# Performance work log

Measured on AMD Instinct MI355X. Metric: run time of the kernel, lower is better.

Reference implementation:

```python
import jax, jax.numpy as jnp
import numpy as np

HIDDEN = 768
HEADS = 12
HEAD_DIM = HIDDEN // HEADS
SCALE = HEAD_DIM ** -0.5
B, S = 8, 1024


def _qkv(x, Wqkv):
    # x: [b, s, H] -> q, k, v each [b, heads, s, d]
    h = jnp.einsum('bsh,hk->bsk', x, Wqkv)          # [b, s, 3*H]
    h = h.reshape(x.shape[0], x.shape[1], 3, HEADS, HEAD_DIM)
    h = jnp.transpose(h, (2, 0, 3, 1, 4))           # [3, b, heads, s, d]
    return h[0], h[1], h[2]


def _attn(q, k, v):
    # q,k,v: [b, heads, s, d]
    att = jax.nn.softmax(jnp.einsum('bhxd,bhyd->bhxy', q, k) * SCALE, axis=-1)
    return jnp.einsum('bhxy,bhyd->bhxd', att, v)


def _out(o, Wout, bout):
    # o: [b, heads, s, d] -> [b, s, H]
    b, h, s, d = o.shape
    o = jnp.transpose(o, (0, 2, 1, 3)).reshape(b, s, h * d)
    return jnp.einsum('bsh,hk->bsk', o, Wout) + bout


def setup_inputs() -> dict:
    key = jax.random.key(0)
    k1, k2, k3, k4, k5 = jax.random.split(key, 5)
    x = jax.random.normal(k1, (B, S, HIDDEN), dtype=jnp.float32)
    x2 = jax.random.normal(k2, (B, S, HIDDEN), dtype=jnp.float32)
    Wqkv = jax.random.normal(k3, (HIDDEN, 3 * HIDDEN), dtype=jnp.float32) * (HIDDEN ** -0.5)
    Wout = jax.random.normal(k4, (HIDDEN, HIDDEN), dtype=jnp.float32) * (HIDDEN ** -0.5)
    bout = jax.random.normal(k5, (HIDDEN,), dtype=jnp.float32) * 0.01
    return {'x': x, 'x2': x2, 'Wqkv': Wqkv, 'Wout': Wout, 'bout': bout}


def reference(x, x2, Wqkv, Wout, bout):
    q, k, v = _qkv(x, Wqkv)
    q2, k2, v2 = _qkv(x2, Wqkv)
    o1 = _attn(q, k, v)      # self-attention on x
    o2 = _attn(q2, k2, v2)   # self-attention on x2
    o3 = _attn(q, k2, v2)    # cross-attention: queries from x, keys/values from x2
    y1 = _out(o1, Wout, bout)
    y2 = _out(o2, Wout, bout)
    y3 = _out(o3, Wout, bout)
    return (y1, y2, y3)
```

## Files before the change

### kernel.cpp

```cpp
#include <hip/hip_runtime.h>
#include <math.h>


#define HIDDEN 768
#define NH 12
#define HD 64
#define BB 8
#define SS 1024
#define ATT_SCALE 0.125f

typedef unsigned short u16;
typedef unsigned int u32;
typedef __attribute__((ext_vector_type(8))) short short8;
typedef __attribute__((ext_vector_type(4))) float f32x4;

constexpr int MROWS = BB * SS;
constexpr int M_QKV = 2 * MROWS;
constexpr int N_QKV = 3 * HIDDEN;
constexpr long QKV_ELEMS = (long)BB * NH * SS * HD;
constexpr long AX_ELEMS  = (long)M_QKV * HIDDEN;
constexpr long O_ELEMS   = (long)3 * MROWS * HIDDEN;
constexpr long WQT_ELEMS = (long)N_QKV * HIDDEN;
constexpr size_t OFF2 = (size_t)12 * QKV_ELEMS * 2;

__device__ inline u16 f2bf(float x) {
    u32 u = __float_as_uint(x);
    return (u16)((u + 0x7FFFu + ((u >> 16) & 1u)) >> 16);
}
__device__ inline float bf2f(u16 h) { return __uint_as_float(((u32)h) << 16); }
__device__ inline int swz(int row, int bcol) {
    return ((row << 7) + bcol) ^ ((row & 7) << 4);
}
__device__ inline int swzV(int row, int bcol) {
    return ((row << 7) + bcol) ^ ((((row >> 3) ^ row) & 7) << 4);
}
#define MFMA16(a, b, c) __builtin_amdgcn_mfma_f32_16x16x32_bf16(a, b, c, 0, 0, 0)

__device__ inline void gload16(const u16* g, u16* l) {
    __builtin_amdgcn_global_load_lds(
        (const __attribute__((address_space(1))) u32*)g,
        (__attribute__((address_space(3))) u32*)l, 16, 0, 0);
}

__global__ __launch_bounds__(256) void conv_x_kernel(
    const float* __restrict__ x, const float* __restrict__ x2,
    u16* __restrict__ axh, u16* __restrict__ axl)
{
    const size_t HALF = (size_t)MROWS * HIDDEN;
    const size_t NTOT = (size_t)AX_ELEMS;
    const size_t step = (size_t)gridDim.x * 256 * 4;
    for (size_t e = ((size_t)blockIdx.x * 256 + threadIdx.x) * 4; e < NTOT; e += step) {
        const float4 v = (e < HALF) ? *(const float4*)&x[e]
                                    : *(const float4*)&x2[e - HALF];
        ushort4 h, l;
        h.x = f2bf(v.x); l.x = f2bf(v.x - bf2f(h.x));
        h.y = f2bf(v.y); l.y = f2bf(v.y - bf2f(h.y));
        h.z = f2bf(v.z); l.z = f2bf(v.z - bf2f(h.z));
        h.w = f2bf(v.w); l.w = f2bf(v.w - bf2f(h.w));
        *(ushort4*)&axh[e] = h;
        *(ushort4*)&axl[e] = l;
    }
}

__global__ __launch_bounds__(256) void conv_wt_kernel(
    const float* __restrict__ Wqkv, const float* __restrict__ Wout,
    u16* __restrict__ wqt_h, u16* __restrict__ wqt_l,
    u16* __restrict__ wot_h, u16* __restrict__ wot_l)
{
    __shared__ float T[64][65];
    const int bk = blockIdx.x;
    int bn = blockIdx.y;
    const float* W; int ncols; u16 *oh, *ol;
    if (bn < 36) { W = Wqkv; ncols = N_QKV; oh = wqt_h; ol = wqt_l; }
    else         { W = Wout; ncols = HIDDEN; oh = wot_h; ol = wot_l; bn -= 36; }
    const int k0 = bk * 64, n0 = bn * 64;
    const int t = threadIdx.x;
    {
        const int r = t >> 2, c0 = (t & 3) * 16;
        #pragma unroll
        for (int q = 0; q < 4; ++q) {
            const float4 v = *(const float4*)&W[(size_t)(k0 + r) * ncols + n0 + c0 + q * 4];
            T[r][c0 + q * 4 + 0] = v.x;
            T[r][c0 + q * 4 + 1] = v.y;
            T[r][c0 + q * 4 + 2] = v.z;
            T[r][c0 + q * 4 + 3] = v.w;
        }
    }
    __syncthreads();
    {
        const int n = t >> 2, kk0 = (t & 3) * 16;
        const size_t ob = (size_t)(n0 + n) * HIDDEN + k0 + kk0;
        #pragma unroll
        for (int q = 0; q < 4; ++q) {
            ushort4 h, l;
            float v0 = T[kk0 + q * 4 + 0][n];
            float v1 = T[kk0 + q * 4 + 1][n];
            float v2 = T[kk0 + q * 4 + 2][n];
            float v3 = T[kk0 + q * 4 + 3][n];
            h.x = f2bf(v0); l.x = f2bf(v0 - bf2f(h.x));
            h.y = f2bf(v1); l.y = f2bf(v1 - bf2f(h.y));
            h.z = f2bf(v2); l.z = f2bf(v2 - bf2f(h.z));
            h.w = f2bf(v3); l.w = f2bf(v3 - bf2f(h.w));
            *(ushort4*)&oh[ob + q * 4] = h;
            *(ushort4*)&ol[ob + q * 4] = l;
        }
    }
}

__global__ __launch_bounds__(256)
__attribute__((amdgpu_waves_per_eu(2, 3)))
void gemm_qkv_mfma(const u16* __restrict__ Agh, const u16* __restrict__ Agl,
                   const u16* __restrict__ Bgh, const u16* __restrict__ Bgl,
                   u16* __restrict__ planes)
{
    __shared__ u16 LAh[4096], LAl[4096], LBh[4096], LBl[4096];

    const int tid = threadIdx.x, lane = tid & 63, wid = tid >> 6;
    const int l15 = lane & 15, lg = lane >> 4;
    const int wr = wid >> 1, wc = wid & 1;
    const int m0 = blockIdx.x * 128, n0 = blockIdx.y * 128;

    const f32x4 fz = {0.f, 0.f, 0.f, 0.f};
    f32x4 acc[4][4] = {{fz,fz,fz,fz},{fz,fz,fz,fz},{fz,fz,fz,fz},{fz,fz,fz,fz}};

    for (int kt = 0; kt < HIDDEN / 32; ++kt) {
        const int k0 = kt * 32;
        __syncthreads();
        #pragma unroll
        for (int u = 0; u < 2; ++u) {
            const int s   = (wid * 2 + u) * 64 + lane;
            const int row = s >> 2;
            const int kc  = (s & 3) * 8;
            const int lo  = (wid * 2 + u) * 512;
            const size_t ga = (size_t)(m0 + row) * HIDDEN + k0 + kc;
            const size_t gb = (size_t)(n0 + row) * HIDDEN + k0 + kc;
            gload16(Agh + ga, &LAh[lo]);
            gload16(Agl + ga, &LAl[lo]);
            gload16(Bgh + gb, &LBh[lo]);
            gload16(Bgl + gb, &LBl[lo]);
        }
        __syncthreads();

        short8 ah[4], al[4], bh[4], bl[4];
        #pragma unroll
        for (int i = 0; i < 4; ++i) {
            const int ro = (wr * 64 + i * 16 + l15) * 32 + lg * 8;
            ah[i] = *(const short8*)&LAh[ro];
            al[i] = *(const short8*)&LAl[ro];
        }
        #pragma unroll
        for (int j = 0; j < 4; ++j) {
            const int ro = (wc * 64 + j * 16 + l15) * 32 + lg * 8;
            bh[j] = *(const short8*)&LBh[ro];
            bl[j] = *(const short8*)&LBl[ro];
        }
        #pragma unroll
        for (int i = 0; i < 4; ++i)
            #pragma unroll
            for (int j = 0; j < 4; ++j) {
                acc[i][j] = MFMA16(ah[i], bh[j], acc[i][j]);
                acc[i][j] = MFMA16(ah[i], bl[j], acc[i][j]);
                acc[i][j] = MFMA16(al[i], bh[j], acc[i][j]);
            }
    }

    #pragma unroll
    for (int i = 0; i < 4; ++i) {
        #pragma unroll
        for (int r = 0; r < 4; ++r) {
            const int mr  = m0 + wr * 64 + i * 16 + lg * 4 + r;
            const int inp = (mr >= MROWS) ? 1 : 0;
            const int mm  = mr & (MROWS - 1);
            const int bb  = mm >> 10, ssr = mm & (SS - 1);
            #pragma unroll
            for (int j = 0; j < 4; ++j) {
                const int n   = n0 + wc * 64 + j * 16 + l15;
                const int sel = n / HIDDEN;
                const int hh  = (n % HIDDEN) >> 6;
                const int dd  = n & 63;
                const float v = acc[i][j][r];
                const u16 vh = f2bf(v);
                const u16 vl = f2bf(v - bf2f(vh));
                u16* ph = planes + (size_t)(inp * 6 + sel * 2) * QKV_ELEMS;
                const size_t idx = (((size_t)bb * NH + hh) * SS + ssr) * HD + dd;
                ph[idx] = vh;
                ph[QKV_ELEMS + idx] = vl;
            }
        }
    }
}

__global__ __launch_bounds__(256)
__attribute__((amdgpu_waves_per_eu(2, 2)))
void attn_mfma_kernel(const u16* __restrict__ planes,
                      u16* __restrict__ o_h, u16* __restrict__ o_l)
{
    __shared__ u16 Khi[64 * 64], Klo[64 * 64];
    __shared__ u16 Vthi[64 * 64], Vtlo[64 * 64];
    __shared__ u16 Pbuf[4][2][2][16 * 64];

    const int tid  = threadIdx.x;
    const int lane = tid & 63, wid = tid >> 6;
    const int l15  = lane & 15, lg = lane >> 4;

    const int work = (blockIdx.x & 7) * 288 + (blockIdx.x >> 3);
    const int qt   = work & 7;
    const int bh   = (work >> 3) % 96;
    const int aid  = (work >> 3) / 96;

    const int qinp  = (aid == 1) ? 1 : 0;
    const int kvinp = (aid == 0) ? 0 : 1;
    const size_t base = (size_t)bh * SS * HD;

    const u16* __restrict__ qhi = planes + (size_t)(qinp * 6 + 0) * QKV_ELEMS;
    const u16* __restrict__ qlo = qhi + QKV_ELEMS;
    const u16* __restrict__ khi = planes + (size_t)(kvinp * 6 + 2) * QKV_ELEMS;
    const u16* __restrict__ klo = khi + QKV_ELEMS;
    const u16* __restrict__ vhi = planes + (size_t)(kvinp * 6 + 4) * QKV_ELEMS;
    const u16* __restrict__ vlo = vhi + QKV_ELEMS;

    const int qb = qt * 128 + wid * 32;
    short8 qfh[2][2], qfl[2][2];
    #pragma unroll
    for (int g = 0; g < 2; ++g)
        #pragma unroll
        for (int dk = 0; dk < 2; ++dk) {
            const size_t off = base + (size_t)(qb + g * 16 + l15) * HD + dk * 32 + lg * 8;
            qfh[g][dk] = *(const short8*)&qhi[off];
            qfl[g][dk] = *(const short8*)&qlo[off];
        }

    const f32x4 fz = {0.f, 0.f, 0.f, 0.f};
    f32x4 O[2][4] = {{fz, fz, fz, fz}, {fz, fz, fz, fz}};
    float mrun[2] = {-INFINITY, -INFINITY};
    float lrun[2] = {0.f, 0.f};

    for (int kt0 = 0; kt0 < SS; kt0 += 64) {
        __syncthreads();
        {
            #pragma unroll
            for (int i = 0; i < 2; ++i) {
                const int c  = tid + 256 * i;
                const int ky = c >> 3, dg = (c & 7) * 8;
                const size_t g = base + (size_t)(kt0 + ky) * HD + dg;
                const int b = swz(ky, dg * 2);
                *(short8*)((char*)Khi + b) = *(const short8*)&khi[g];
                *(short8*)((char*)Klo + b) = *(const short8*)&klo[g];
            }
            const int kp = tid >> 3;
            const int d0 = (tid & 7) * 8;
            const size_t g0 = base + (size_t)(kt0 + 2 * kp) * HD + d0;
            short8 vah = *(const short8*)&vhi[g0];
            short8 vbh = *(const short8*)&vhi[g0 + HD];
            short8 val = *(const short8*)&vlo[g0];
            short8 vbl = *(const short8*)&vlo[g0 + HD];
            #pragma unroll
            for (int i = 0; i < 8; ++i) {
                const int d = d0 + i;
                const int b = swzV(d, kp * 4);
                *(u32*)((char*)Vthi + b) = (u32)(u16)vah[i] | ((u32)(u16)vbh[i] << 16);
                *(u32*)((char*)Vtlo + b) = (u32)(u16)val[i] | ((u32)(u16)vbl[i] << 16);
            }
        }
        __syncthreads();

        f32x4 S[2][4] = {{fz, fz, fz, fz}, {fz, fz, fz, fz}};
        #pragma unroll
        for (int dk = 0; dk < 2; ++dk) {
            #pragma unroll
            for (int kt = 0; kt < 4; ++kt) {
                const int b = swz(kt * 16 + l15, dk * 64 + lg * 16);
                short8 kfh = *(const short8*)((char*)Khi + b);
                short8 kfl = *(const short8*)((char*)Klo + b);
                #pragma unroll
                for (int g = 0; g < 2; ++g) {
                    S[g][kt] = MFMA16(kfh, qfh[g][dk], S[g][kt]);
                    S[g][kt] = MFMA16(kfl, qfh[g][dk], S[g][kt]);
                    S[g][kt] = MFMA16(kfh, qfl[g][dk], S[g][kt]);
                }
            }
        }

        #pragma unroll
        for (int g = 0; g < 2; ++g) {
            float pm = -INFINITY;
            #pragma unroll
            for (int kt = 0; kt < 4; ++kt)
                #pragma unroll
                for (int r = 0; r < 4; ++r) {
                    S[g][kt][r] *= ATT_SCALE;
                    pm = fmaxf(pm, S[g][kt][r]);
                }
            pm = fmaxf(pm, __shfl_xor(pm, 16, 64));
            pm = fmaxf(pm, __shfl_xor(pm, 32, 64));

            if (__any(pm - mrun[g] > 8.f)) {
                const float mnew = fmaxf(mrun[g], pm);
                const float corr = __expf(mrun[g] - mnew);
                lrun[g] *= corr;
                #pragma unroll
                for (int r = 0; r < 4; ++r) {
                    const float c = __shfl(corr, lg * 4 + r, 64);
                    #pragma unroll
                    for (int dn = 0; dn < 4; ++dn) O[g][dn][r] *= c;
                }
                mrun[g] = mnew;
            }
            const float mref = mrun[g];

            u16* __restrict__ Ph = &Pbuf[wid][g][0][0];
            u16* __restrict__ Pl = &Pbuf[wid][g][1][0];
            float psum = 0.f;
            #pragma unroll
            for (int kt = 0; kt < 4; ++kt) {
                float p0 = __expf(S[g][kt][0] - mref);
                float p1 = __expf(S[g][kt][1] - mref);
                float p2 = __expf(S[g][kt][2] - mref);
                float p3 = __expf(S[g][kt][3] - mref);
                psum += (p0 + p1) + (p2 + p3);
                const u32 u0 = __float_as_uint(p0), u1 = __float_as_uint(p1);
                const u32 u2 = __float_as_uint(p2), u3 = __float_as_uint(p3);
                const u32 hpk0 = (u0 >> 16) | (u1 & 0xFFFF0000u);
                const u32 hpk1 = (u2 >> 16) | (u3 & 0xFFFF0000u);
                const float l0 = p0 - __uint_as_float(u0 & 0xFFFF0000u);
                const float l1 = p1 - __uint_as_float(u1 & 0xFFFF0000u);
                const float l2 = p2 - __uint_as_float(u2 & 0xFFFF0000u);
                const float l3 = p3 - __uint_as_float(u3 & 0xFFFF0000u);
                const u32 lpk0 = (__float_as_uint(l0) >> 16) | (__float_as_uint(l1) & 0xFFFF0000u);
                const u32 lpk1 = (__float_as_uint(l2) >> 16) | (__float_as_uint(l3) & 0xFFFF0000u);
                const int b0 = swz(l15, kt * 32 + lg * 8);
                *(uint2*)((char*)Ph + b0) = make_uint2(hpk0, hpk1);
                *(uint2*)((char*)Pl + b0) = make_uint2(lpk0, lpk1);
            }
            psum += __shfl_xor(psum, 16, 64);
            psum += __shfl_xor(psum, 32, 64);
            lrun[g] += psum;
        }

        #pragma unroll
        for (int ch = 0; ch < 2; ++ch) {
            short8 vfh[4], vfl[4];
            #pragma unroll
            for (int dn = 0; dn < 4; ++dn) {
                const int vb = swzV(dn * 16 + l15, ch * 64 + lg * 16);
                vfh[dn] = *(const short8*)((char*)Vthi + vb);
                vfl[dn] = *(const short8*)((char*)Vtlo + vb);
            }
            #pragma unroll
            for (int g = 0; g < 2; ++g) {
                const int pb = swz(l15, ch * 64 + lg * 16);
                short8 pah = *(const short8*)((char*)&Pbuf[wid][g][0][0] + pb);
                short8 pal = *(const short8*)((char*)&Pbuf[wid][g][1][0] + pb);
                #pragma unroll
                for (int dn = 0; dn < 4; ++dn) {
                    O[g][dn] = MFMA16(pah, vfh[dn], O[g][dn]);
                    O[g][dn] = MFMA16(pah, vfl[dn], O[g][dn]);
                    O[g][dn] = MFMA16(pal, vfh[dn], O[g][dn]);
                }
            }
        }
    }

    const int b = bh / NH, h = bh % NH;
    #pragma unroll
    for (int g = 0; g < 2; ++g) {
        const float linv = 1.f / lrun[g];
        #pragma unroll
        for (int r = 0; r < 4; ++r) {
            const float inv = __shfl(linv, lg * 4 + r, 64);
            const int grow = aid * MROWS + b * SS + qb + g * 16 + lg * 4 + r;
            const size_t rb = (size_t)grow * HIDDEN + h * HD;
            #pragma unroll
            for (int dn = 0; dn < 4; ++dn) {
                const float v = O[g][dn][r] * inv;
                const u16 vh = f2bf(v);
                o_h[rb + dn * 16 + l15] = vh;
                o_l[rb + dn * 16 + l15] = f2bf(v - bf2f(vh));
            }
        }
    }
}

__global__ __launch_bounds__(256)
__attribute__((amdgpu_waves_per_eu(2, 3)))
void gemm_out_mfma(const u16* __restrict__ Agh, const u16* __restrict__ Agl,
                   const u16* __restrict__ Bgh, const u16* __restrict__ Bgl,
                   const float* __restrict__ bias, float* __restrict__ out)
{
    __shared__ u16 LAh[4096], LAl[4096], LBh[4096], LBl[4096];

    const int tid = threadIdx.x, lane = tid & 63, wid = tid >> 6;
    const int l15 = lane & 15, lg = lane >> 4;
    const int wr = wid >> 1, wc = wid & 1;
    const int m0 = blockIdx.x * 128, n0 = blockIdx.y * 128;

    const f32x4 fz = {0.f, 0.f, 0.f, 0.f};
    f32x4 acc[4][4] = {{fz,fz,fz,fz},{fz,fz,fz,fz},{fz,fz,fz,fz},{fz,fz,fz,fz}};

    for (int kt = 0; kt < HIDDEN / 32; ++kt) {
        const int k0 = kt * 32;
        __syncthreads();
        #pragma unroll
        for (int u = 0; u < 2; ++u) {
            const int s   = (wid * 2 + u) * 64 + lane;
            const int row = s >> 2;
            const int kc  = (s & 3) * 8;
            const int lo  = (wid * 2 + u) * 512;
            const size_t ga = (size_t)(m0 + row) * HIDDEN + k0 + kc;
            const size_t gb = (size_t)(n0 + row) * HIDDEN + k0 + kc;
            gload16(Agh + ga, &LAh[lo]);
            gload16(Agl + ga, &LAl[lo]);
            gload16(Bgh + gb, &LBh[lo]);
            gload16(Bgl + gb, &LBl[lo]);
        }
        __syncthreads();

        short8 ah[4], al[4], bh[4], bl[4];
        #pragma unroll
        for (int i = 0; i < 4; ++i) {
            const int ro = (wr * 64 + i * 16 + l15) * 32 + lg * 8;
            ah[i] = *(const short8*)&LAh[ro];
            al[i] = *(const short8*)&LAl[ro];
        }
        #pragma unroll
        for (int j = 0; j < 4; ++j) {
            const int ro = (wc * 64 + j * 16 + l15) * 32 + lg * 8;
            bh[j] = *(const short8*)&LBh[ro];
            bl[j] = *(const short8*)&LBl[ro];
        }
        #pragma unroll
        for (int i = 0; i < 4; ++i)
            #pragma unroll
            for (int j = 0; j < 4; ++j) {
                acc[i][j] = MFMA16(ah[i], bh[j], acc[i][j]);
                acc[i][j] = MFMA16(ah[i], bl[j], acc[i][j]);
                acc[i][j] = MFMA16(al[i], bh[j], acc[i][j]);
            }
    }

    #pragma unroll
    for (int i = 0; i < 4; ++i) {
        #pragma unroll
        for (int r = 0; r < 4; ++r) {
            const int mr = m0 + wr * 64 + i * 16 + lg * 4 + r;
            #pragma unroll
            for (int j = 0; j < 4; ++j) {
                const int n = n0 + wc * 64 + j * 16 + l15;
                out[(size_t)mr * HIDDEN + n] = acc[i][j][r] + bias[n];
            }
        }
    }
}

extern "C" void kernel_launch(void* const* d_in, const int* in_sizes, int n_in,
                              void* d_out, int out_size, void* d_ws, size_t ws_size,
                              hipStream_t stream)
{
    const float* x    = (const float*)d_in[0];
    const float* x2   = (const float*)d_in[1];
    const float* Wqkv = (const float*)d_in[2];
    const float* Wout = (const float*)d_in[3];
    const float* bout = (const float*)d_in[4];
    float* out = (float*)d_out;

    char* wsb = (char*)d_ws;
    u16* planes = (u16*)wsb;
    u16* ax_h  = (u16*)(wsb + OFF2);
    u16* ax_l  = ax_h + AX_ELEMS;
    u16* wqt_h = ax_l + AX_ELEMS;
    u16* wqt_l = wqt_h + WQT_ELEMS;
    u16* o_h   = (u16*)(wsb + OFF2);
    u16* o_l   = o_h + O_ELEMS;
    u16* wot_h = o_l + O_ELEMS;
    u16* wot_l = wot_h + (long)HIDDEN * HIDDEN;

    conv_x_kernel<<<3072, 256, 0, stream>>>(x, x2, ax_h, ax_l);

    dim3 gw(12, 48);
    conv_wt_kernel<<<gw, 256, 0, stream>>>(Wqkv, Wout, wqt_h, wqt_l, wot_h, wot_l);

    dim3 g1(M_QKV / 128, N_QKV / 128);
    gemm_qkv_mfma<<<g1, 256, 0, stream>>>(ax_h, ax_l, wqt_h, wqt_l, planes);

    attn_mfma_kernel<<<2304, 256, 0, stream>>>(planes, o_h, o_l);

    dim3 g3(3 * MROWS / 128, HIDDEN / 128);
    gemm_out_mfma<<<g3, 256, 0, stream>>>(o_h, o_l, wot_h, wot_l, bout, out);
}
```

Measured before the change: 659.3 us.

## Reuse K shared buffers for P tiles and raise attention occupancy

Drops the separate per-wave P staging buffer and writes the probability tiles into the K hi/lo shared arrays once the QK^T MFMAs are done, which needs an extra barrier. This cuts LDS per block and raises the waves-per-EU target from 2 to 4-5. The PV loop is reorganised per query group with V fragments loaded inside it, and MFMA sections are wrapped in s_setprio. The tighter register budget may cause spills, and reloading V fragments adds LDS traffic.

```diff
diff --git a/kernel.cpp b/kernel.cpp
--- a/kernel.cpp
+++ b/kernel.cpp
@@ -191,13 +191,12 @@
 }
 
 __global__ __launch_bounds__(256)
-__attribute__((amdgpu_waves_per_eu(2, 2)))
+__attribute__((amdgpu_waves_per_eu(4, 5)))
 void attn_mfma_kernel(const u16* __restrict__ planes,
                       u16* __restrict__ o_h, u16* __restrict__ o_l)
 {
     __shared__ u16 Khi[64 * 64], Klo[64 * 64];
     __shared__ u16 Vthi[64 * 64], Vtlo[64 * 64];
-    __shared__ u16 Pbuf[4][2][2][16 * 64];
 
     const int tid  = threadIdx.x;
     const int lane = tid & 63, wid = tid >> 6;
@@ -265,6 +264,7 @@
         __syncthreads();
 
         f32x4 S[2][4] = {{fz, fz, fz, fz}, {fz, fz, fz, fz}};
+        __builtin_amdgcn_s_setprio(1);
         #pragma unroll
         for (int dk = 0; dk < 2; ++dk) {
             #pragma unroll
@@ -280,6 +280,8 @@
                 }
             }
         }
+        __builtin_amdgcn_s_setprio(0);
+        __syncthreads();
 
         #pragma unroll
         for (int g = 0; g < 2; ++g) {
@@ -308,8 +310,7 @@
             }
             const float mref = mrun[g];
 
-            u16* __restrict__ Ph = &Pbuf[wid][g][0][0];
-            u16* __restrict__ Pl = &Pbuf[wid][g][1][0];
+            const int prow = wid * 16 + l15;
             float psum = 0.f;
             #pragma unroll
             for (int kt = 0; kt < 4; ++kt) {
@@ -328,36 +329,31 @@
                 const float l3 = p3 - __uint_as_float(u3 & 0xFFFF0000u);
                 const u32 lpk0 = (__float_as_uint(l0) >> 16) | (__float_as_uint(l1) & 0xFFFF0000u);
                 const u32 lpk1 = (__float_as_uint(l2) >> 16) | (__float_as_uint(l3) & 0xFFFF0000u);
-                const int b0 = swz(l15, kt * 32 + lg * 8);
-                *(uint2*)((char*)Ph + b0) = make_uint2(hpk0, hpk1);
-                *(uint2*)((char*)Pl + b0) = make_uint2(lpk0, lpk1);
+                const int b0 = swz(prow, kt * 32 + lg * 8);
+                *(uint2*)((char*)Khi + b0) = make_uint2(hpk0, hpk1);
+                *(uint2*)((char*)Klo + b0) = make_uint2(lpk0, lpk1);
             }
             psum += __shfl_xor(psum, 16, 64);
             psum += __shfl_xor(psum, 32, 64);
             lrun[g] += psum;
-        }
-
-        #pragma unroll
-        for (int ch = 0; ch < 2; ++ch) {
-            short8 vfh[4], vfl[4];
-            #pragma unroll
-            for (int dn = 0; dn < 4; ++dn) {
-                const int vb = swzV(dn * 16 + l15, ch * 64 + lg * 16);
-                vfh[dn] = *(const short8*)((char*)Vthi + vb);
-                vfl[dn] = *(const short8*)((char*)Vtlo + vb);
-            }
-            #pragma unroll
-            for (int g = 0; g < 2; ++g) {
-                const int pb = swz(l15, ch * 64 + lg * 16);
-                short8 pah = *(const short8*)((char*)&Pbuf[wid][g][0][0] + pb);
-                short8 pal = *(const short8*)((char*)&Pbuf[wid][g][1][0] + pb);
+
+            __builtin_amdgcn_s_setprio(1);
+            #pragma unroll
+            for (int ch = 0; ch < 2; ++ch) {
+                const int pb = swz(prow, ch * 64 + lg * 16);
+                short8 pah = *(const short8*)((char*)Khi + pb);
+                short8 pal = *(const short8*)((char*)Klo + pb);
                 #pragma unroll
                 for (int dn = 0; dn < 4; ++dn) {
-                    O[g][dn] = MFMA16(pah, vfh[dn], O[g][dn]);
-                    O[g][dn] = MFMA16(pah, vfl[dn], O[g][dn]);
-                    O[g][dn] = MFMA16(pal, vfh[dn], O[g][dn]);
+                    const int vb = swzV(dn * 16 + l15, ch * 64 + lg * 16);
+                    short8 vfh = *(const short8*)((char*)Vthi + vb);
+                    short8 vfl = *(const short8*)((char*)Vtlo + vb);
+                    O[g][dn] = MFMA16(pah, vfh, O[g][dn]);
+                    O[g][dn] = MFMA16(pah, vfl, O[g][dn]);
+                    O[g][dn] = MFMA16(pal, vfh, O[g][dn]);
                 }
             }
+            __builtin_amdgcn_s_setprio(0);
         }
     }
 
```

Result: slower. 836.3 us (+26.8%).
